# Kernel tuning notes

Measured on AMD Instinct MI355X. Metric: run time of the kernel, lower is better.

Reference implementation:

```python
import jax, jax.numpy as jnp
import numpy as np

HEADS = 4
A_DIMS = 64
V_DIMS = 64
NODES_NUM = 128
F_DIMS = 256
LN_EPS = 1e-5


def setup_inputs() -> dict:
    key = jax.random.key(0)
    ks = jax.random.split(key, 7)
    b, n = 8, 8192
    x = jax.random.normal(ks[0], (b, n, F_DIMS), dtype=jnp.float32)
    nodes = jax.random.normal(ks[1], (NODES_NUM, A_DIMS), dtype=jnp.float32)
    Wa = jax.random.normal(ks[2], (F_DIMS, A_DIMS * HEADS), dtype=jnp.float32) * (F_DIMS ** -0.5)
    Wv = jax.random.normal(ks[3], (F_DIMS, V_DIMS * HEADS), dtype=jnp.float32) * (F_DIMS ** -0.5)
    bv = jax.random.normal(ks[4], (V_DIMS * HEADS,), dtype=jnp.float32) * 0.02
    gamma = jnp.ones((V_DIMS * HEADS,), dtype=jnp.float32)
    beta = jnp.zeros((V_DIMS * HEADS,), dtype=jnp.float32)
    return {"x": x, "nodes": nodes, "Wa": Wa, "Wv": Wv, "bv": bv, "gamma": gamma, "beta": beta}


def reference(x, nodes, Wa, Wv, bv, gamma, beta):
    b, n, d = x.shape
    scale = A_DIMS ** -0.5
    # projections: (b, n, h*d) -> (b, h, n, d)
    a = (x @ Wa).reshape(b, n, HEADS, A_DIMS).transpose(0, 2, 1, 3)
    v = (x @ Wv + bv).reshape(b, n, HEADS, V_DIMS).transpose(0, 2, 1, 3)
    # learned-query cross attention: nodes shared across heads
    attn = jnp.einsum('id,bhjd->bhij', nodes, a) * scale  # (b, h, nodes, n)
    attn = jax.nn.softmax(attn, axis=-1)
    out = jnp.einsum('bhij,bhjd->bhid', attn, v)  # (b, h, nodes, v)
    out = out.transpose(0, 2, 1, 3).reshape(b, NODES_NUM, HEADS * V_DIMS)
    out = jnp.where(out >= 0, out, 0.2 * out)  # leaky_relu(0.2)
    mu = jnp.mean(out, axis=-1, keepdims=True)
    var = jnp.mean((out - mu) ** 2, axis=-1, keepdims=True)
    out = (out - mu) * jax.lax.rsqrt(var + LN_EPS) * gamma + beta
    return out
```

## Files before the change

### kernel.cpp

```cpp
#include <hip/hip_runtime.h>
#include <math.h>

typedef float f32x4 __attribute__((ext_vector_type(4)));
typedef short s16x8 __attribute__((ext_vector_type(8)));
typedef unsigned short u16;
typedef u16 u16x4 __attribute__((ext_vector_type(4)));
typedef unsigned int u32;

#define NCH 8
#define NT  32

__device__ __forceinline__ u16 f2bf(float f){
  union { float f; u32 u; } v; v.f = f;
  u32 r = v.u + 0x7FFFu + ((v.u >> 16) & 1u);
  return (u16)(r >> 16);
}
__device__ __forceinline__ float bf2f(u16 b){
  union { u32 u; float f; } v; v.u = ((u32)b) << 16; return v.f;
}
__device__ __forceinline__ f32x4 mfma16(s16x8 a, s16x8 b, f32x4 c){
  return __builtin_amdgcn_mfma_f32_16x16x32_bf16(a, b, c, 0, 0, 0);
}

__global__ __launch_bounds__(256) void k0_cvt(const float* __restrict__ x,
                                              u16* __restrict__ xbf, u16* __restrict__ xT){
  __shared__ u16 T[64*68];
  const int tid = threadIdx.x;
  const int bx = blockIdx.x;
  const int b = bx >> 9, rest = bx & 511, jt = rest >> 2, ft = rest & 3;
  const float* xp = x + (long)b*2097152 + (long)jt*16384 + ft*64;
  u16* xbp = xbf + (long)b*2097152 + (long)jt*16384 + ft*64;
  #pragma unroll
  for (int p=0;p<4;++p){
    int e = p*1024 + tid*4;
    int row = e >> 6, f = e & 63;
    float4 v = *(const float4*)(xp + (long)row*256 + f);
    u16x4 u = { f2bf(v.x), f2bf(v.y), f2bf(v.z), f2bf(v.w) };
    *(u16x4*)(xbp + (long)row*256 + f) = u;
    *(u16x4*)&T[row*68 + f] = u;
  }
  __syncthreads();
  u16* xtp = xT + (long)b*2097152 + (long)(ft*64)*8192 + (long)jt*64;
  #pragma unroll
  for (int p=0;p<4;++p){
    int e = p*1024 + tid*4;
    int fr = e >> 6, j = e & 63;
    u16x4 u = { T[j*68 + fr], T[(j+1)*68 + fr], T[(j+2)*68 + fr], T[(j+3)*68 + fr] };
    *(u16x4*)(xtp + (long)fr*8192 + j) = u;
  }
}

__global__ __launch_bounds__(256) void k1_q(const float* __restrict__ nodes,
    const float* __restrict__ Wa, u16* __restrict__ Qbf){
  __shared__ float nd[64];
  const int bx = blockIdx.x;
  const int h = bx >> 7, i = bx & 127;
  const int tid = threadIdx.x;
  if (tid < 64) nd[tid] = nodes[i*64 + tid];
  __syncthreads();
  const float* wp = Wa + tid*256 + h*64;
  float acc = 0.f;
  #pragma unroll
  for (int d=0; d<64; d+=4){
    float4 wv = *(const float4*)(wp + d);
    acc += nd[d]*wv.x + nd[d+1]*wv.y + nd[d+2]*wv.z + nd[d+3]*wv.w;
  }
  Qbf[(h*128 + i)*256 + tid] = f2bf(acc * 0.125f);
}

__global__ __launch_bounds__(256,2) void k2_attn(const u16* __restrict__ xbf,
    const u16* __restrict__ xT, const u16* __restrict__ Qbf,
    u16* __restrict__ ctxp, float* __restrict__ stats){
  __shared__ u16 Xs[32*264];
  __shared__ u16 XTs[256*40];
  __shared__ u16 Pl[64*40];
  __shared__ float flds[64];

  const int tid = threadIdx.x;
  const int l = tid & 63, w = tid >> 6;
  const int li = l & 15, g = l >> 4;
  const int nbL = w * 16;

  const int idx = blockIdx.x;
  const int q  = idx & 63;
  const int hh = idx >> 6;
  const int h = hh & 3, half = hh >> 2;
  const int b = q >> 3, ch = q & 7;
  const int nodeG = half*64 + nbL;

  s16x8 qf[8];
  #pragma unroll
  for (int kf=0; kf<8; ++kf)
    qf[kf] = *(const s16x8*)(Qbf + ((h*128 + nodeG + li)*256 + kf*32 + g*8));

  f32x4 cacc[16];
  #pragma unroll
  for (int ff=0;ff<16;++ff){ f32x4 z = {0.f,0.f,0.f,0.f}; cacc[ff] = z; }

  float m0 = -INFINITY, ls0 = 0.f;

  const u16* xb  = xbf + (long)b*2097152 + (long)ch*262144;
  const u16* xtb = xT  + (long)b*2097152 + (long)ch*1024;

  s16x8 pXs[4], pXT[4];
  #pragma unroll
  for (int p=0;p<4;++p){
    pXs[p] = *(const s16x8*)(xb + (long)(p*8 + (tid>>5))*256 + (tid&31)*8);
    pXT[p] = *(const s16x8*)(xtb + (long)(p*64 + (tid>>2))*8192 + (tid&3)*8);
  }

  for (int tt=0; tt<NT; ++tt){
    __syncthreads();
    #pragma unroll
    for (int p=0;p<4;++p){
      *(s16x8*)&Xs[(p*8 + (tid>>5))*264 + (tid&31)*8] = pXs[p];
      *(s16x8*)&XTs[(p*64 + (tid>>2))*40 + (tid&3)*8] = pXT[p];
    }
    if (tt+1 < NT){
      const long jb = (long)(tt+1)*32;
      #pragma unroll
      for (int p=0;p<4;++p){
        pXs[p] = *(const s16x8*)(xb + (jb + p*8 + (tid>>5))*256 + (tid&31)*8);
        pXT[p] = *(const s16x8*)(xtb + (long)(p*64 + (tid>>2))*8192 + jb + (tid&3)*8);
      }
    }
    __syncthreads();

    f32x4 s00={0.f,0.f,0.f,0.f}, s10={0.f,0.f,0.f,0.f};
    #pragma unroll
    for (int kf=0; kf<8; ++kf){
      s16x8 ax0 = *(const s16x8*)&Xs[li*264 + kf*32 + g*8];
      s16x8 ax1 = *(const s16x8*)&Xs[(16+li)*264 + kf*32 + g*8];
      s00 = mfma16(ax0, qf[kf], s00);
      s10 = mfma16(ax1, qf[kf], s10);
    }

    float t0 = fmaxf(fmaxf(fmaxf(s00[0],s00[1]),fmaxf(s00[2],s00[3])),
                     fmaxf(fmaxf(s10[0],s10[1]),fmaxf(s10[2],s10[3])));
    t0 = fmaxf(t0, __shfl_xor(t0,16)); t0 = fmaxf(t0, __shfl_xor(t0,32));
    float mn0 = fmaxf(m0,t0);
    float fac0 = __expf(m0-mn0);
    #pragma unroll
    for (int rr=0;rr<4;++rr){
      s00[rr]=__expf(s00[rr]-mn0); s10[rr]=__expf(s10[rr]-mn0);
    }
    float u0 = s00[0]+s00[1]+s00[2]+s00[3] + s10[0]+s10[1]+s10[2]+s10[3];
    ls0 = ls0*fac0 + u0;
    const bool nochange = __all(fac0==1.0f);
    m0 = mn0;

    {
      u16x4 p00 = { f2bf(s00[0]),f2bf(s00[1]),f2bf(s00[2]),f2bf(s00[3]) };
      u16x4 p10 = { f2bf(s10[0]),f2bf(s10[1]),f2bf(s10[2]),f2bf(s10[3]) };
      *(u16x4*)&Pl[(nbL+li)*40 + g*4]      = p00;
      *(u16x4*)&Pl[(nbL+li)*40 + 16 + g*4] = p10;
    }
    if (g==0){ flds[nbL+li] = fac0; }

    if (!nochange){
      float fr0[4];
      #pragma unroll
      for (int rr=0;rr<4;++rr){ fr0[rr] = flds[nbL + g*4 + rr]; }
      #pragma unroll
      for (int ff=0; ff<16; ++ff)
        #pragma unroll
        for (int rr=0;rr<4;++rr){ cacc[ff][rr]*=fr0[rr]; }
    }

    s16x8 pa0 = *(const s16x8*)&Pl[(nbL+li)*40 + g*8];
    #pragma unroll
    for (int ff=0; ff<16; ++ff){
      s16x8 bx = *(const s16x8*)&XTs[(ff*16+li)*40 + g*8];
      cacc[ff] = mfma16(pa0, bx, cacc[ff]);
    }
  }

  ls0 += __shfl_xor(ls0,16); ls0 += __shfl_xor(ls0,32);
  const int sb = ((b*4 + h)*NCH + ch)*128;
  if (g==0){
    stats[2*(sb + nodeG + li)    ] = m0;
    stats[2*(sb + nodeG + li) + 1] = ls0;
  }
  u16* cp = ctxp + (long)sb*256;
  #pragma unroll
  for (int ff=0;ff<16;++ff)
    #pragma unroll
    for (int rr=0;rr<4;++rr){
      int node = nodeG + g*4 + rr;
      int f = ff*16 + li;
      cp[(long)node*256 + f] = f2bf(cacc[ff][rr]);
    }
}

__global__ __launch_bounds__(256) void k3_out(const u16* __restrict__ ctxp,
    const float* __restrict__ stats, const float* __restrict__ Wv,
    const float* __restrict__ bv, const float* __restrict__ gamma,
    const float* __restrict__ beta, float* __restrict__ out){
  __shared__ float ctxL[4*256];
  __shared__ float red[8];
  const int tid = threadIdx.x;
  const int bx = blockIdx.x;
  const int b = bx >> 7, node = bx & 127;
  #pragma unroll
  for (int h=0; h<4; ++h){
    float mc[NCH], lc[NCH];
    #pragma unroll
    for (int c=0;c<NCH;++c){
      int si = ((b*4+h)*NCH + c)*128 + node;
      mc[c] = stats[2*si]; lc[c] = stats[2*si+1];
    }
    float mm = mc[0];
    #pragma unroll
    for (int c=1;c<NCH;++c) mm = fmaxf(mm, mc[c]);
    float L = 0.f, acc = 0.f;
    #pragma unroll
    for (int c=0;c<NCH;++c){
      float wc = __expf(mc[c]-mm);
      L += wc*lc[c];
      acc += wc * bf2f(ctxp[((long)((b*4+h)*NCH + c)*128 + node)*256 + tid]);
    }
    ctxL[h*256 + tid] = acc / L;
  }
  __syncthreads();
  const int hh = tid >> 6;
  float o = bv[tid];
  const float* cx = &ctxL[hh*256];
  #pragma unroll 8
  for (int f=0; f<256; ++f) o = fmaf(cx[f], Wv[f*256 + tid], o);
  o = (o >= 0.f) ? o : 0.2f*o;
  float s1 = o, s2 = o*o;
  #pragma unroll
  for (int d=1; d<64; d<<=1){ s1 += __shfl_xor(s1,d); s2 += __shfl_xor(s2,d); }
  if ((tid&63)==0){ red[tid>>6] = s1; red[4 + (tid>>6)] = s2; }
  __syncthreads();
  float S1 = red[0]+red[1]+red[2]+red[3];
  float S2 = red[4]+red[5]+red[6]+red[7];
  float mu = S1 * (1.f/256.f);
  float var = S2 * (1.f/256.f) - mu*mu;
  float rs = rsqrtf(fmaxf(var, 0.f) + 1e-5f);
  out[(long)(b*128 + node)*256 + tid] = (o - mu)*rs*gamma[tid] + beta[tid];
}

extern "C" void kernel_launch(void* const* d_in, const int* in_sizes, int n_in,
                              void* d_out, int out_size, void* d_ws, size_t ws_size,
                              hipStream_t stream){
  const float* x     = (const float*)d_in[0];
  const float* nodes = (const float*)d_in[1];
  const float* Wa    = (const float*)d_in[2];
  const float* Wv    = (const float*)d_in[3];
  const float* bv    = (const float*)d_in[4];
  const float* gamma = (const float*)d_in[5];
  const float* beta  = (const float*)d_in[6];
  float* out = (float*)d_out;

  u16* xbf  = (u16*)d_ws;
  u16* xT   = xbf + 16777216;
  u16* Qbf  = xT + 16777216;
  u16* ctxp = Qbf + 131072;
  float* stats = (float*)(ctxp + 8388608);

  k0_cvt<<<dim3(4096), dim3(256), 0, stream>>>(x, xbf, xT);
  k1_q  <<<dim3(512),  dim3(256), 0, stream>>>(nodes, Wa, Qbf);
  k2_attn<<<dim3(512), dim3(256), 0, stream>>>(xbf, xT, Qbf, ctxp, stats);
  k3_out<<<dim3(1024), dim3(256), 0, stream>>>(ctxp, stats, Wv, bv, gamma, beta, out);
}
```

Baseline: 113.7 us.

## Double-buffer attention tiles in LDS and unroll loop by two

Splits the LDS tiles for X and X^T into two buffers and unrolls the tile loop by two, so each iteration needs one barrier instead of two while register prefetches run two tiles ahead. The per-row rescale factor now travels by wavefront shuffle instead of through shared memory, and the occupancy hint in the launch bounds is dropped. This doubles LDS use and register prefetch state, which may lower occupancy. The Pl buffer is still shared between successive compute stages with no barrier around it, though each wave appears to use only its own rows.

```diff
diff --git a/kernel.cpp b/kernel.cpp
--- a/kernel.cpp
+++ b/kernel.cpp
@@ -68,13 +68,12 @@
   Qbf[(h*128 + i)*256 + tid] = f2bf(acc * 0.125f);
 }
 
-__global__ __launch_bounds__(256,2) void k2_attn(const u16* __restrict__ xbf,
+__global__ __launch_bounds__(256) void k2_attn(const u16* __restrict__ xbf,
     const u16* __restrict__ xT, const u16* __restrict__ Qbf,
     u16* __restrict__ ctxp, float* __restrict__ stats){
-  __shared__ u16 Xs[32*264];
-  __shared__ u16 XTs[256*40];
+  __shared__ u16 Xs0[32*264], Xs1[32*264];
+  __shared__ u16 XT0[256*40], XT1[256*40];
   __shared__ u16 Pl[64*40];
-  __shared__ float flds[64];
 
   const int tid = threadIdx.x;
   const int l = tid & 63, w = tid >> 6;
@@ -102,77 +101,78 @@
   const u16* xb  = xbf + (long)b*2097152 + (long)ch*262144;
   const u16* xtb = xT  + (long)b*2097152 + (long)ch*1024;
 
-  s16x8 pXs[4], pXT[4];
-  #pragma unroll
-  for (int p=0;p<4;++p){
-    pXs[p] = *(const s16x8*)(xb + (long)(p*8 + (tid>>5))*256 + (tid&31)*8);
-    pXT[p] = *(const s16x8*)(xtb + (long)(p*64 + (tid>>2))*8192 + (tid&3)*8);
-  }
-
-  for (int tt=0; tt<NT; ++tt){
+#define PREFETCH(PXS, PXT, JB) \
+  _Pragma("unroll") \
+  for (int p=0;p<4;++p){ \
+    PXS[p] = *(const s16x8*)(xb + (size_t)((JB) + p*8 + (tid>>5))*256 + (tid&31)*8); \
+    PXT[p] = *(const s16x8*)(xtb + (size_t)(p*64 + (tid>>2))*8192 + (JB) + (tid&3)*8); \
+  }
+
+#define STAGE_WRITE(XS, XTS, PXS, PXT) \
+  _Pragma("unroll") \
+  for (int p=0;p<4;++p){ \
+    *(s16x8*)&XS[(p*8 + (tid>>5))*264 + (tid&31)*8] = PXS[p]; \
+    *(s16x8*)&XTS[(p*64 + (tid>>2))*40 + (tid&3)*8] = PXT[p]; \
+  }
+
+#define COMPUTE(XS, XTS) { \
+    f32x4 s00={0.f,0.f,0.f,0.f}, s10={0.f,0.f,0.f,0.f}; \
+    _Pragma("unroll") \
+    for (int kf=0; kf<8; ++kf){ \
+      s16x8 ax0 = *(const s16x8*)&XS[li*264 + kf*32 + g*8]; \
+      s16x8 ax1 = *(const s16x8*)&XS[(16+li)*264 + kf*32 + g*8]; \
+      s00 = mfma16(ax0, qf[kf], s00); \
+      s10 = mfma16(ax1, qf[kf], s10); \
+    } \
+    float t0 = fmaxf(fmaxf(fmaxf(s00[0],s00[1]),fmaxf(s00[2],s00[3])), \
+                     fmaxf(fmaxf(s10[0],s10[1]),fmaxf(s10[2],s10[3]))); \
+    t0 = fmaxf(t0, __shfl_xor(t0,16)); t0 = fmaxf(t0, __shfl_xor(t0,32)); \
+    float mn0 = fmaxf(m0,t0); \
+    float fac0 = __expf(m0-mn0); \
+    _Pragma("unroll") \
+    for (int rr=0;rr<4;++rr){ \
+      s00[rr]=__expf(s00[rr]-mn0); s10[rr]=__expf(s10[rr]-mn0); \
+    } \
+    float u0 = s00[0]+s00[1]+s00[2]+s00[3] + s10[0]+s10[1]+s10[2]+s10[3]; \
+    ls0 = ls0*fac0 + u0; \
+    const bool nochange = __all(fac0==1.0f); \
+    m0 = mn0; \
+    { \
+      u16x4 p00 = { f2bf(s00[0]),f2bf(s00[1]),f2bf(s00[2]),f2bf(s00[3]) }; \
+      u16x4 p10 = { f2bf(s10[0]),f2bf(s10[1]),f2bf(s10[2]),f2bf(s10[3]) }; \
+      *(u16x4*)&Pl[(nbL+li)*40 + g*4]      = p00; \
+      *(u16x4*)&Pl[(nbL+li)*40 + 16 + g*4] = p10; \
+    } \
+    if (!nochange){ \
+      float fr0[4]; \
+      _Pragma("unroll") \
+      for (int rr=0;rr<4;++rr){ fr0[rr] = __shfl(fac0, nbL? (g*4+rr) : (g*4+rr)); } \
+      _Pragma("unroll") \
+      for (int ff=0; ff<16; ++ff) \
+        _Pragma("unroll") \
+        for (int rr=0;rr<4;++rr){ cacc[ff][rr]*=fr0[rr]; } \
+    } \
+    s16x8 pa0 = *(const s16x8*)&Pl[(nbL+li)*40 + g*8]; \
+    _Pragma("unroll") \
+    for (int ff=0; ff<16; ++ff){ \
+      s16x8 bx = *(const s16x8*)&XTS[(ff*16+li)*40 + g*8]; \
+      cacc[ff] = mfma16(pa0, bx, cacc[ff]); \
+    } \
+  }
+
+  s16x8 pXsA[4], pXTA[4], pXsB[4], pXTB[4];
+  PREFETCH(pXsA, pXTA, 0);
+  PREFETCH(pXsB, pXTB, 32);
+
+  for (int tt=0; tt<NT; tt+=2){
+    STAGE_WRITE(Xs0, XT0, pXsA, pXTA);
     __syncthreads();
-    #pragma unroll
-    for (int p=0;p<4;++p){
-      *(s16x8*)&Xs[(p*8 + (tid>>5))*264 + (tid&31)*8] = pXs[p];
-      *(s16x8*)&XTs[(p*64 + (tid>>2))*40 + (tid&3)*8] = pXT[p];
-    }
-    if (tt+1 < NT){
-      const long jb = (long)(tt+1)*32;
-      #pragma unroll
-      for (int p=0;p<4;++p){
-        pXs[p] = *(const s16x8*)(xb + (jb + p*8 + (tid>>5))*256 + (tid&31)*8);
-        pXT[p] = *(const s16x8*)(xtb + (long)(p*64 + (tid>>2))*8192 + jb + (tid&3)*8);
-      }
-    }
+    if (tt+2 < NT) PREFETCH(pXsA, pXTA, (tt+2)*32);
+    COMPUTE(Xs0, XT0);
+    STAGE_WRITE(Xs1, XT1, pXsB, pXTB);
     __syncthreads();
-
-    f32x4 s00={0.f,0.f,0.f,0.f}, s10={0.f,0.f,0.f,0.f};
-    #pragma unroll
-    for (int kf=0; kf<8; ++kf){
-      s16x8 ax0 = *(const s16x8*)&Xs[li*264 + kf*32 + g*8];
-      s16x8 ax1 = *(const s16x8*)&Xs[(16+li)*264 + kf*32 + g*8];
-      s00 = mfma16(ax0, qf[kf], s00);
-      s10 = mfma16(ax1, qf[kf], s10);
-    }
-
-    float t0 = fmaxf(fmaxf(fmaxf(s00[0],s00[1]),fmaxf(s00[2],s00[3])),
-                     fmaxf(fmaxf(s10[0],s10[1]),fmaxf(s10[2],s10[3])));
-    t0 = fmaxf(t0, __shfl_xor(t0,16)); t0 = fmaxf(t0, __shfl_xor(t0,32));
-    float mn0 = fmaxf(m0,t0);
-    float fac0 = __expf(m0-mn0);
-    #pragma unroll
-    for (int rr=0;rr<4;++rr){
-      s00[rr]=__expf(s00[rr]-mn0); s10[rr]=__expf(s10[rr]-mn0);
-    }
-    float u0 = s00[0]+s00[1]+s00[2]+s00[3] + s10[0]+s10[1]+s10[2]+s10[3];
-    ls0 = ls0*fac0 + u0;
-    const bool nochange = __all(fac0==1.0f);
-    m0 = mn0;
-
-    {
-      u16x4 p00 = { f2bf(s00[0]),f2bf(s00[1]),f2bf(s00[2]),f2bf(s00[3]) };
-      u16x4 p10 = { f2bf(s10[0]),f2bf(s10[1]),f2bf(s10[2]),f2bf(s10[3]) };
-      *(u16x4*)&Pl[(nbL+li)*40 + g*4]      = p00;
-      *(u16x4*)&Pl[(nbL+li)*40 + 16 + g*4] = p10;
-    }
-    if (g==0){ flds[nbL+li] = fac0; }
-
-    if (!nochange){
-      float fr0[4];
-      #pragma unroll
-      for (int rr=0;rr<4;++rr){ fr0[rr] = flds[nbL + g*4 + rr]; }
-      #pragma unroll
-      for (int ff=0; ff<16; ++ff)
-        #pragma unroll
-        for (int rr=0;rr<4;++rr){ cacc[ff][rr]*=fr0[rr]; }
-    }
-
-    s16x8 pa0 = *(const s16x8*)&Pl[(nbL+li)*40 + g*8];
-    #pragma unroll
-    for (int ff=0; ff<16; ++ff){
-      s16x8 bx = *(const s16x8*)&XTs[(ff*16+li)*40 + g*8];
-      cacc[ff] = mfma16(pa0, bx, cacc[ff]);
-    }
+    if (tt+3 < NT) PREFETCH(pXsB, pXTB, (tt+3)*32);
+    COMPUTE(Xs1, XT1);
   }
 
   ls0 += __shfl_xor(ls0,16); ls0 += __shfl_xor(ls0,32);
```

Result: slower. 147.3 us (+29.5%).

## Drop row-major bf16 copy of x; convert fp32 in attention kernel

Applied to the files above, without the earlier changes.

The conversion kernel no longer writes a row-major bf16 copy of x. The attention kernel instead loads fp32 x directly and packs it to bf16 with v_cvt_pk_bf16_f32 before storing to shared memory. This removes a 32 MB write and its later read-back, but doubles the bytes read per tile in the attention kernel, since each of the 8 head/half blocks rereads fp32 x. The shared-memory flds exchange of rescale factors is replaced with wave shuffles, and the prefetch now starts after the second barrier.

```diff
diff --git a/kernel.cpp b/kernel.cpp
--- a/kernel.cpp
+++ b/kernel.cpp
@@ -6,6 +6,7 @@
 typedef unsigned short u16;
 typedef u16 u16x4 __attribute__((ext_vector_type(4)));
 typedef unsigned int u32;
+typedef u32 u32x4 __attribute__((ext_vector_type(4)));
 
 #define NCH 8
 #define NT  32
@@ -21,22 +22,25 @@
 __device__ __forceinline__ f32x4 mfma16(s16x8 a, s16x8 b, f32x4 c){
   return __builtin_amdgcn_mfma_f32_16x16x32_bf16(a, b, c, 0, 0, 0);
 }
+__device__ __forceinline__ u32 pk_bf16(float lo, float hi){
+  u32 r;
+  asm("v_cvt_pk_bf16_f32 %0, %1, %2" : "=v"(r) : "v"(lo), "v"(hi));
+  return r;
+}
 
 __global__ __launch_bounds__(256) void k0_cvt(const float* __restrict__ x,
-                                              u16* __restrict__ xbf, u16* __restrict__ xT){
+                                              u16* __restrict__ xT){
   __shared__ u16 T[64*68];
   const int tid = threadIdx.x;
   const int bx = blockIdx.x;
   const int b = bx >> 9, rest = bx & 511, jt = rest >> 2, ft = rest & 3;
   const float* xp = x + (long)b*2097152 + (long)jt*16384 + ft*64;
-  u16* xbp = xbf + (long)b*2097152 + (long)jt*16384 + ft*64;
   #pragma unroll
   for (int p=0;p<4;++p){
     int e = p*1024 + tid*4;
     int row = e >> 6, f = e & 63;
     float4 v = *(const float4*)(xp + (long)row*256 + f);
     u16x4 u = { f2bf(v.x), f2bf(v.y), f2bf(v.z), f2bf(v.w) };
-    *(u16x4*)(xbp + (long)row*256 + f) = u;
     *(u16x4*)&T[row*68 + f] = u;
   }
   __syncthreads();
@@ -68,13 +72,12 @@
   Qbf[(h*128 + i)*256 + tid] = f2bf(acc * 0.125f);
 }
 
-__global__ __launch_bounds__(256,2) void k2_attn(const u16* __restrict__ xbf,
+__global__ __launch_bounds__(256,2) void k2_attn(const float* __restrict__ x,
     const u16* __restrict__ xT, const u16* __restrict__ Qbf,
     u16* __restrict__ ctxp, float* __restrict__ stats){
   __shared__ u16 Xs[32*264];
   __shared__ u16 XTs[256*40];
   __shared__ u16 Pl[64*40];
-  __shared__ float flds[64];
 
   const int tid = threadIdx.x;
   const int l = tid & 63, w = tid >> 6;
@@ -99,32 +102,44 @@
 
   float m0 = -INFINITY, ls0 = 0.f;
 
-  const u16* xb  = xbf + (long)b*2097152 + (long)ch*262144;
-  const u16* xtb = xT  + (long)b*2097152 + (long)ch*1024;
-
-  s16x8 pXs[4], pXT[4];
+  const float* xbF = x  + (long)b*2097152 + (long)ch*262144;
+  const u16*   xtb = xT + (long)b*2097152 + (long)ch*1024;
+
+  float4 pf[8];
+  s16x8 pXT[4];
   #pragma unroll
   for (int p=0;p<4;++p){
-    pXs[p] = *(const s16x8*)(xb + (long)(p*8 + (tid>>5))*256 + (tid&31)*8);
-    pXT[p] = *(const s16x8*)(xtb + (long)(p*64 + (tid>>2))*8192 + (tid&3)*8);
+    const float* src = xbF + (size_t)(p*8 + (tid>>5))*256 + (tid&31)*8;
+    pf[2*p]   = *(const float4*)(src);
+    pf[2*p+1] = *(const float4*)(src + 4);
+    pXT[p] = *(const s16x8*)(xtb + (size_t)(p*64 + (tid>>2))*8192 + (tid&3)*8);
   }
 
   for (int tt=0; tt<NT; ++tt){
     __syncthreads();
+
     #pragma unroll
     for (int p=0;p<4;++p){
-      *(s16x8*)&Xs[(p*8 + (tid>>5))*264 + (tid&31)*8] = pXs[p];
+      u32x4 vv = { pk_bf16(pf[2*p].x,   pf[2*p].y),
+                   pk_bf16(pf[2*p].z,   pf[2*p].w),
+                   pk_bf16(pf[2*p+1].x, pf[2*p+1].y),
+                   pk_bf16(pf[2*p+1].z, pf[2*p+1].w) };
+      *(u32x4*)&Xs[(p*8 + (tid>>5))*264 + (tid&31)*8] = vv;
       *(s16x8*)&XTs[(p*64 + (tid>>2))*40 + (tid&3)*8] = pXT[p];
     }
+
+    __syncthreads();
+
     if (tt+1 < NT){
-      const long jb = (long)(tt+1)*32;
+      const size_t jb = (size_t)(tt+1)*32;
       #pragma unroll
       for (int p=0;p<4;++p){
-        pXs[p] = *(const s16x8*)(xb + (jb + p*8 + (tid>>5))*256 + (tid&31)*8);
-        pXT[p] = *(const s16x8*)(xtb + (long)(p*64 + (tid>>2))*8192 + jb + (tid&3)*8);
+        const float* src = xbF + (jb + p*8 + (tid>>5))*256 + (tid&31)*8;
+        pf[2*p]   = *(const float4*)(src);
+        pf[2*p+1] = *(const float4*)(src + 4);
+        pXT[p] = *(const s16x8*)(xtb + (size_t)(p*64 + (tid>>2))*8192 + jb + (tid&3)*8);
       }
     }
-    __syncthreads();
 
     f32x4 s00={0.f,0.f,0.f,0.f}, s10={0.f,0.f,0.f,0.f};
     #pragma unroll
@@ -155,12 +170,11 @@
       *(u16x4*)&Pl[(nbL+li)*40 + g*4]      = p00;
       *(u16x4*)&Pl[(nbL+li)*40 + 16 + g*4] = p10;
     }
-    if (g==0){ flds[nbL+li] = fac0; }
 
     if (!nochange){
       float fr0[4];
       #pragma unroll
-      for (int rr=0;rr<4;++rr){ fr0[rr] = flds[nbL + g*4 + rr]; }
+      for (int rr=0;rr<4;++rr){ fr0[rr] = __shfl(fac0, g*4 + rr); }
       #pragma unroll
       for (int ff=0; ff<16; ++ff)
         #pragma unroll
@@ -253,14 +267,13 @@
   const float* beta  = (const float*)d_in[6];
   float* out = (float*)d_out;
 
-  u16* xbf  = (u16*)d_ws;
-  u16* xT   = xbf + 16777216;
+  u16* xT   = (u16*)d_ws;
   u16* Qbf  = xT + 16777216;
   u16* ctxp = Qbf + 131072;
   float* stats = (float*)(ctxp + 8388608);
 
-  k0_cvt<<<dim3(4096), dim3(256), 0, stream>>>(x, xbf, xT);
+  k0_cvt<<<dim3(4096), dim3(256), 0, stream>>>(x, xT);
   k1_q  <<<dim3(512),  dim3(256), 0, stream>>>(nodes, Wa, Qbf);
-  k2_attn<<<dim3(512), dim3(256), 0, stream>>>(xbf, xT, Qbf, ctxp, stats);
+  k2_attn<<<dim3(512), dim3(256), 0, stream>>>(x, xT, Qbf, ctxp, stats);
   k3_out<<<dim3(1024), dim3(256), 0, stream>>>(ctxp, stats, Wv, bv, gamma, beta, out);
 }
```

New measurement: 108.8 us (median of 3 runs). -4.3%, faster.

## Load X score operands directly into registers, bypass LDS staging

Applied to the files above, without the earlier changes.

The X tile feeding the score MFMAs is now loaded from global memory straight into per-lane register fragments (16 s16x8 per thread) and prefetched one tile ahead, instead of being staged through shared memory. The per-row rescale factor is broadcast with a wavefront shuffle instead of an LDS array. This cuts LDS traffic and shared memory footprint but each wave now loads the X tile redundantly from global/L2 and register pressure rises under the 2-blocks-per-SM launch bound.

```diff
diff --git a/kernel.cpp b/kernel.cpp
--- a/kernel.cpp
+++ b/kernel.cpp
@@ -71,10 +71,8 @@
 __global__ __launch_bounds__(256,2) void k2_attn(const u16* __restrict__ xbf,
     const u16* __restrict__ xT, const u16* __restrict__ Qbf,
     u16* __restrict__ ctxp, float* __restrict__ stats){
-  __shared__ u16 Xs[32*264];
   __shared__ u16 XTs[256*40];
   __shared__ u16 Pl[64*40];
-  __shared__ float flds[64];
 
   const int tid = threadIdx.x;
   const int l = tid & 63, w = tid >> 6;
@@ -102,37 +100,46 @@
   const u16* xb  = xbf + (long)b*2097152 + (long)ch*262144;
   const u16* xtb = xT  + (long)b*2097152 + (long)ch*1024;
 
-  s16x8 pXs[4], pXT[4];
-  #pragma unroll
-  for (int p=0;p<4;++p){
-    pXs[p] = *(const s16x8*)(xb + (long)(p*8 + (tid>>5))*256 + (tid&31)*8);
-    pXT[p] = *(const s16x8*)(xtb + (long)(p*64 + (tid>>2))*8192 + (tid&3)*8);
-  }
+  s16x8 xq0[8], xq1[8], pXT[4];
+  #pragma unroll
+  for (int kf=0; kf<8; ++kf){
+    xq0[kf] = *(const s16x8*)(xb + (size_t)li*256       + kf*32 + g*8);
+    xq1[kf] = *(const s16x8*)(xb + (size_t)(16+li)*256  + kf*32 + g*8);
+  }
+  #pragma unroll
+  for (int p=0;p<4;++p)
+    pXT[p] = *(const s16x8*)(xtb + (size_t)(p*64 + (tid>>2))*8192 + (tid&3)*8);
 
   for (int tt=0; tt<NT; ++tt){
     __syncthreads();
-    #pragma unroll
-    for (int p=0;p<4;++p){
-      *(s16x8*)&Xs[(p*8 + (tid>>5))*264 + (tid&31)*8] = pXs[p];
+
+    #pragma unroll
+    for (int p=0;p<4;++p)
       *(s16x8*)&XTs[(p*64 + (tid>>2))*40 + (tid&3)*8] = pXT[p];
-    }
+
+    __syncthreads();
+
     if (tt+1 < NT){
-      const long jb = (long)(tt+1)*32;
-      #pragma unroll
-      for (int p=0;p<4;++p){
-        pXs[p] = *(const s16x8*)(xb + (jb + p*8 + (tid>>5))*256 + (tid&31)*8);
-        pXT[p] = *(const s16x8*)(xtb + (long)(p*64 + (tid>>2))*8192 + jb + (tid&3)*8);
+      const size_t jb = (size_t)(tt+1)*32;
+      #pragma unroll
+      for (int p=0;p<4;++p)
+        pXT[p] = *(const s16x8*)(xtb + (size_t)(p*64 + (tid>>2))*8192 + jb + (tid&3)*8);
+    }
+
+    f32x4 s00={0.f,0.f,0.f,0.f}, s10={0.f,0.f,0.f,0.f};
+    #pragma unroll
+    for (int kf=0; kf<8; ++kf){
+      s00 = mfma16(xq0[kf], qf[kf], s00);
+      s10 = mfma16(xq1[kf], qf[kf], s10);
+    }
+
+    if (tt+1 < NT){
+      const size_t jb = (size_t)(tt+1)*32;
+      #pragma unroll
+      for (int kf=0; kf<8; ++kf){
+        xq0[kf] = *(const s16x8*)(xb + (jb+li)*256      + kf*32 + g*8);
+        xq1[kf] = *(const s16x8*)(xb + (jb+16+li)*256   + kf*32 + g*8);
       }
-    }
-    __syncthreads();
-
-    f32x4 s00={0.f,0.f,0.f,0.f}, s10={0.f,0.f,0.f,0.f};
-    #pragma unroll
-    for (int kf=0; kf<8; ++kf){
-      s16x8 ax0 = *(const s16x8*)&Xs[li*264 + kf*32 + g*8];
-      s16x8 ax1 = *(const s16x8*)&Xs[(16+li)*264 + kf*32 + g*8];
-      s00 = mfma16(ax0, qf[kf], s00);
-      s10 = mfma16(ax1, qf[kf], s10);
     }
 
     float t0 = fmaxf(fmaxf(fmaxf(s00[0],s00[1]),fmaxf(s00[2],s00[3])),
@@ -155,12 +162,11 @@
       *(u16x4*)&Pl[(nbL+li)*40 + g*4]      = p00;
       *(u16x4*)&Pl[(nbL+li)*40 + 16 + g*4] = p10;
     }
-    if (g==0){ flds[nbL+li] = fac0; }
 
     if (!nochange){
       float fr0[4];
       #pragma unroll
-      for (int rr=0;rr<4;++rr){ fr0[rr] = flds[nbL + g*4 + rr]; }
+      for (int rr=0;rr<4;++rr){ fr0[rr] = __shfl(fac0, g*4 + rr); }
       #pragma unroll
       for (int ff=0; ff<16; ++ff)
         #pragma unroll
```

Result: slower. 179.4 us (+57.7%).
